# Optimization experiments

Measured on AMD Instinct MI355X. Metric: run time of the kernel, lower is better.

Reference implementation:

```python
import jax, jax.numpy as jnp
from jax import lax
import numpy as np

B, W, M, F = 8, 20, 512, 16
H = 128          # n_hidden
HALF = 64        # half_hid
K = 10           # conv out channels
LONG_K = W // 2  # dilated conv kernel


def setup_inputs() -> dict:
    key = jax.random.key(0)
    ks = jax.random.split(key, 24)
    s = 0.1  # weight scale (xavier-ish)
    return {
        "X": jax.random.normal(ks[0], (B, W, M, F), jnp.float32),
        "Y": jax.random.uniform(ks[1], (B, M), jnp.float32),
        "adj": jax.random.uniform(ks[2], (M, M), jnp.float32),
        "V": jax.random.normal(ks[3], (HALF,), jnp.float32) * s,
        "bv": jax.random.normal(ks[4], (1,), jnp.float32) * s,
        "W1": jax.random.normal(ks[5], (HALF, H), jnp.float32) * s,
        "b1": jax.random.normal(ks[6], (HALF,), jnp.float32) * s,
        "W2": jax.random.normal(ks[7], (HALF, H), jnp.float32) * s,
        "Wb": jax.random.normal(ks[8], (M, M), jnp.float32) * s,
        "wb": jax.random.normal(ks[9], (1,), jnp.float32) * s,
        "conv_w": jax.random.normal(ks[10], (K, F, W), jnp.float32) * s,
        "conv_b": jax.random.normal(ks[11], (K,), jnp.float32) * s,
        "convl_w": jax.random.normal(ks[12], (K, F, LONG_K), jnp.float32) * s,
        "convl_b": jax.random.normal(ks[13], (K,), jnp.float32) * s,
        "gru_Wih": jax.random.normal(ks[14], (3 * H, F), jnp.float32) * s,
        "gru_Whh": jax.random.normal(ks[15], (3 * H, H), jnp.float32) * s,
        "gru_bih": jax.random.normal(ks[16], (3 * H,), jnp.float32) * s,
        "gru_bhh": jax.random.normal(ks[17], (3 * H,), jnp.float32) * s,
        "gc1_W": jax.random.normal(ks[18], (3 * K, H), jnp.float32) * s,
        "gc1_b": jax.random.normal(ks[19], (H,), jnp.float32) * s,
        "gc2_W": jax.random.normal(ks[20], (H, K), jnp.float32) * s,
        "gc2_b": jax.random.normal(ks[21], (K,), jnp.float32) * s,
        "out_W": jax.random.normal(ks[22], (1, H + K), jnp.float32) * s,
        "out_b": jax.random.normal(ks[23], (1,), jnp.float32) * s,
    }


def _gru_last(xseq, Wih, Whh, bih, bhh):
    # xseq: (N, T, F) -> last hidden (N, H), PyTorch GRU gate order r,z,n
    n_hid = Whh.shape[1]
    def step(h, x_t):
        gx = x_t @ Wih.T + bih
        gh = h @ Whh.T + bhh
        xr, xz, xn = jnp.split(gx, 3, axis=-1)
        hr, hz, hn = jnp.split(gh, 3, axis=-1)
        r = jax.nn.sigmoid(xr + hr)
        z = jax.nn.sigmoid(xz + hz)
        n = jnp.tanh(xn + r * hn)
        return (1.0 - z) * n + z * h, None
    h0 = jnp.zeros((xseq.shape[0], n_hid), xseq.dtype)
    hT, _ = lax.scan(step, h0, jnp.moveaxis(xseq, 1, 0))
    return hT


def _forward(X, Y, adj, V, bv, W1, b1, W2, Wb, wb, conv_w, conv_b, convl_w,
             convl_b, gru_Wih, gru_Whh, gru_bih, gru_bhh, gc1_W, gc1_b,
             gc2_W, gc2_b, out_W, out_b):
    b, w, m, f = X.shape
    # ---- temporal branch: GRU per node ----
    x = jnp.transpose(X, (0, 2, 1, 3)).reshape(b * m, w, f)
    last_hid = _gru_last(x, gru_Wih, gru_Whh, gru_bih, gru_bhh).reshape(b, m, -1)
    out_temporal = last_hid
    # ---- attention-style adaptive adjacency ----
    # hid_rpt_m[b,i,j]=last_hid[b,j]; hid_rpt_w[b,i,j]=last_hid[b,i]
    p1 = jnp.einsum('bjh,kh->bjk', last_hid, W1)  # pairs with column index j
    p2 = jnp.einsum('bih,kh->bik', last_hid, W2)  # pairs with row index i
    pre = p1[:, None, :, :] + p2[:, :, None, :] + b1  # (b,m,m,half)
    a_mx = jnp.einsum('bijk,k->bij', jax.nn.elu(pre), V) + bv[0]
    # F.normalize(p=2, dim=1)
    nrm = jnp.sqrt(jnp.sum(a_mx * a_mx, axis=1, keepdims=True))
    a_mx = a_mx / jnp.maximum(nrm, 1e-12)
    # ---- per-node conv1d (vectorized over nodes) ----
    Xc = jnp.transpose(X, (0, 2, 3, 1)).reshape(b * m, f, w)  # (bm, f, w)
    dn = ('NCH', 'OIH', 'NCH')
    r = lax.conv_general_dilated(Xc, conv_w, (1,), 'VALID', dimension_numbers=dn)
    r = r + conv_b[None, :, None]                      # (bm, K, 1)
    rl = lax.conv_general_dilated(Xc, convl_w, (1,), 'VALID',
                                  rhs_dilation=(2,), dimension_numbers=dn)
    rl = rl + convl_b[None, :, None]                   # (bm, K, long_out)
    r_cat = jnp.concatenate([r, rl], axis=-1)          # (bm, K, 1+long_out)
    r_l = jax.nn.relu(r_cat.reshape(b, m, -1))         # (b, m, (1+long_out)*K)
    # ---- gate learned adjacency with fixed adjacency ----
    c = jax.nn.sigmoid(jnp.einsum('bij,jk->bik', a_mx, Wb) + wb[0])
    A = adj[None] * c + a_mx * (1.0 - c)               # (b,m,m)
    # ---- graph convolutions: out = A @ (x @ W) + b ----
    h1 = jax.nn.relu(jnp.einsum('bij,bjh->bih', A, r_l @ gc1_W) + gc1_b)
    out_spatial = jax.nn.relu(jnp.einsum('bij,bjh->bih', A, h1 @ gc2_W) + gc2_b)
    # ---- readout ----
    out = jnp.concatenate([out_spatial, out_temporal], axis=-1)
    out = (out @ out_W.T + out_b).squeeze(-1)          # (b, m)
    y = out.reshape(-1)
    Yf = Y.reshape(-1)
    # BCE with logits: softplus(y) - Y*y, averaged
    loss = jnp.mean(jax.nn.softplus(y) - Yf * y)
    return loss, jax.nn.sigmoid(y)


def reference(X, Y, adj, V, bv, W1, b1, W2, Wb, wb, conv_w, conv_b, convl_w,
              convl_b, gru_Wih, gru_Whh, gru_bih, gru_bhh, gc1_W, gc1_b,
              gc2_W, gc2_b, out_W, out_b):
    return _forward(X, Y, adj, V, bv, W1, b1, W2, Wb, wb, conv_w, conv_b,
                    convl_w, convl_b, gru_Wih, gru_Whh, gru_bih, gru_bhh,
                    gc1_W, gc1_b, gc2_W, gc2_b, out_W, out_b)
```

## Files before the change

kernel.cpp:

```cpp
#include <hip/hip_runtime.h>
#include <math.h>

#define Bn 8
#define Wn 20
#define Mn 512
#define Fn 16
#define Hn 128

typedef __attribute__((ext_vector_type(8))) short short8;
typedef __attribute__((ext_vector_type(4))) float f32x4;
typedef unsigned short ushort_t;

__device__ __forceinline__ float sigmoidf_(float x) {
  return 1.0f / (1.0f + __expf(-x));
}
__device__ __forceinline__ float tanhf_(float x) {
  float xx = fminf(fmaxf(x, -15.f), 15.f);
  float e = __expf(2.f * xx);
  return (e - 1.f) / (e + 1.f);
}
__device__ __forceinline__ float reluf_(float x) { return fmaxf(x, 0.f); }
__device__ __forceinline__ float eluf_(float x) {
  return (x > 0.f) ? x : (__expf(x) - 1.f);
}
__device__ __forceinline__ ushort_t bf16_rne(float v) {
  unsigned u = __float_as_uint(v);
  u += 0x7FFFu + ((u >> 16) & 1u);
  return (ushort_t)(u >> 16);
}
__device__ __forceinline__ float bf16_to_f(ushort_t b) {
  return __uint_as_float(((unsigned)b) << 16);
}
__device__ __forceinline__ void split8(const float v[8], short8& hi, short8& lo) {
#pragma unroll
  for (int j = 0; j < 8; ++j) {
    ushort_t h = bf16_rne(v[j]);
    hi[j] = (short)h;
    lo[j] = (short)bf16_rne(v[j] - bf16_to_f(h));
  }
}
__device__ __forceinline__ void load_gate_frags(
    const float* __restrict__ Whh, const float* __restrict__ Wih,
    int row, int quad, short8 fr[5][2]) {
  const float* wrow = Whh + (long)row * 128;
#pragma unroll
  for (int ks = 0; ks < 4; ++ks) {
    float v[8];
    float4 a4 = *(const float4*)&wrow[ks * 32 + quad * 8];
    float4 b4 = *(const float4*)&wrow[ks * 32 + quad * 8 + 4];
    v[0] = a4.x; v[1] = a4.y; v[2] = a4.z; v[3] = a4.w;
    v[4] = b4.x; v[5] = b4.y; v[6] = b4.z; v[7] = b4.w;
    split8(v, fr[ks][0], fr[ks][1]);
  }
  {
    float v[8] = {0.f, 0.f, 0.f, 0.f, 0.f, 0.f, 0.f, 0.f};
    if (quad < 2) {
      const float* xrow = Wih + (long)row * 16;
      float4 a4 = *(const float4*)&xrow[quad * 8];
      float4 b4 = *(const float4*)&xrow[quad * 8 + 4];
      v[0] = a4.x; v[1] = a4.y; v[2] = a4.z; v[3] = a4.w;
      v[4] = b4.x; v[5] = b4.y; v[6] = b4.z; v[7] = b4.w;
    }
    split8(v, fr[4][0], fr[4][1]);
  }
}

#define LDK 168
#define HSZ (16 * LDK)
__global__ __launch_bounds__(512, 1) void gru_kernel(
    const float* __restrict__ X, const float* __restrict__ Whh,
    const float* __restrict__ Wih, const float* __restrict__ bih,
    const float* __restrict__ bhh, const float* __restrict__ W1,
    const float* __restrict__ W2, const float* __restrict__ b1,
    float* __restrict__ last_hid, float* __restrict__ p1,
    float* __restrict__ p2, float* __restrict__ ssq,
    float* __restrict__ d_out) {
  const int tid = threadIdx.x;
  const int wave = tid >> 6;
  const int lane = tid & 63;
  const int quad = lane >> 4;
  const int jl = lane & 15;
  const int j0 = wave * 16;
  const int blk = blockIdx.x;
  const int b = blk >> 5;
  const int m0 = (blk & 31) * 16;

  if (blk < 8) ssq[blk * 512 + tid] = 0.f;
  if (blk == 0 && tid == 0) d_out[0] = 0.f;

  __shared__ __align__(16) ushort_t smem_hs[4 * HSZ];

  short8 frR[5][2], frZ[5][2], frN[5][2];
  load_gate_frags(Whh, Wih, wave * 16 + jl, quad, frR);
  load_gate_frags(Whh, Wih, 128 + wave * 16 + jl, quad, frZ);
  load_gate_frags(Whh, Wih, 256 + wave * 16 + jl, quad, frN);

  const float cr  = bih[j0 + jl] + bhh[j0 + jl];
  const float cz  = bih[128 + j0 + jl] + bhh[128 + j0 + jl];
  const float cnx = bih[256 + j0 + jl];
  const float cnh = bhh[256 + j0 + jl];

  for (int i = tid; i < 4 * HSZ; i += 512) smem_hs[i] = 0;

  const float* Xb = X + (long)b * (Wn * Mn * Fn) + (long)m0 * Fn;
  float x0 = 0.f;
  if (tid < 256) x0 = Xb[tid];
  __syncthreads();
  if (tid < 256) {
    int s = tid >> 4, f = tid & 15;
    ushort_t hb = bf16_rne(x0);
    smem_hs[0 * HSZ + s * LDK + 128 + f] = hb;
    smem_hs[2 * HSZ + s * LDK + 128 + f] = bf16_rne(x0 - bf16_to_f(hb));
  }
  __syncthreads();

  float hp[4] = {0.f, 0.f, 0.f, 0.f};

  for (int t = 0; t < Wn; ++t) {
    const int cur = t & 1, nxt = cur ^ 1;
    const int hiC = cur * HSZ, loC = (2 + cur) * HSZ;
    const int hiN = nxt * HSZ, loN = (2 + nxt) * HSZ;
    float xpre = 0.f;
    if (tid < 256 && t < Wn - 1) xpre = Xb[(long)(t + 1) * (Mn * Fn) + tid];

    f32x4 aR[2], aZ[2], aHN[2], aXN;
    aR[0] = aR[1] = aZ[0] = aZ[1] = aHN[0] = aHN[1] = aXN = (f32x4){0.f, 0.f, 0.f, 0.f};
#pragma unroll
    for (int ks = 0; ks < 5; ++ks) {
      const int p = ks & 1;
      short8 ah = *(const short8*)&smem_hs[hiC + jl * LDK + ks * 32 + quad * 8];
      short8 al = *(const short8*)&smem_hs[loC + jl * LDK + ks * 32 + quad * 8];
      aR[p] = __builtin_amdgcn_mfma_f32_16x16x32_bf16(ah, frR[ks][0], aR[p], 0, 0, 0);
      aR[p] = __builtin_amdgcn_mfma_f32_16x16x32_bf16(ah, frR[ks][1], aR[p], 0, 0, 0);
      aR[p] = __builtin_amdgcn_mfma_f32_16x16x32_bf16(al, frR[ks][0], aR[p], 0, 0, 0);
      aZ[p] = __builtin_amdgcn_mfma_f32_16x16x32_bf16(ah, frZ[ks][0], aZ[p], 0, 0, 0);
      aZ[p] = __builtin_amdgcn_mfma_f32_16x16x32_bf16(ah, frZ[ks][1], aZ[p], 0, 0, 0);
      aZ[p] = __builtin_amdgcn_mfma_f32_16x16x32_bf16(al, frZ[ks][0], aZ[p], 0, 0, 0);
      if (ks < 4) {
        aHN[p] = __builtin_amdgcn_mfma_f32_16x16x32_bf16(ah, frN[ks][0], aHN[p], 0, 0, 0);
        aHN[p] = __builtin_amdgcn_mfma_f32_16x16x32_bf16(ah, frN[ks][1], aHN[p], 0, 0, 0);
        aHN[p] = __builtin_amdgcn_mfma_f32_16x16x32_bf16(al, frN[ks][0], aHN[p], 0, 0, 0);
      } else {
        aXN = __builtin_amdgcn_mfma_f32_16x16x32_bf16(ah, frN[4][0], aXN, 0, 0, 0);
        aXN = __builtin_amdgcn_mfma_f32_16x16x32_bf16(ah, frN[4][1], aXN, 0, 0, 0);
        aXN = __builtin_amdgcn_mfma_f32_16x16x32_bf16(al, frN[4][0], aXN, 0, 0, 0);
      }
    }

#pragma unroll
    for (int reg = 0; reg < 4; ++reg) {
      float r = sigmoidf_(aR[0][reg] + aR[1][reg] + cr);
      float z = sigmoidf_(aZ[0][reg] + aZ[1][reg] + cz);
      float n = tanhf_(aXN[reg] + cnx + r * (aHN[0][reg] + aHN[1][reg] + cnh));
      float h = (1.f - z) * n + z * hp[reg];
      hp[reg] = h;
      int s = quad * 4 + reg;
      ushort_t hb = bf16_rne(h);
      smem_hs[hiN + s * LDK + j0 + jl] = hb;
      smem_hs[loN + s * LDK + j0 + jl] = bf16_rne(h - bf16_to_f(hb));
    }
    if (tid < 256 && t < Wn - 1) {
      int s = tid >> 4, f = tid & 15;
      ushort_t hb = bf16_rne(xpre);
      smem_hs[hiN + s * LDK + 128 + f] = hb;
      smem_hs[loN + s * LDK + 128 + f] = bf16_rne(xpre - bf16_to_f(hb));
    }
    __syncthreads();
  }

  float* hs_f = (float*)smem_hs;
#pragma unroll
  for (int reg = 0; reg < 4; ++reg) {
    int s = quad * 4 + reg;
    float h = hp[reg];
    last_hid[(long)(blk * 16 + s) * Hn + j0 + jl] = h;
    hs_f[s * 132 + j0 + jl] = h;
  }
  __syncthreads();
  {
    int k = tid & 63;
    int part = (tid >> 6) & 1;
    int sg = tid >> 7;
    const float* Wp = part ? W2 : W1;
    float a[4];
    float init = part ? 0.f : b1[k];
    a[0] = a[1] = a[2] = a[3] = init;
    for (int h = 0; h < 128; h += 4) {
      float4 w = *(const float4*)&Wp[k * 128 + h];
#pragma unroll
      for (int rr = 0; rr < 4; ++rr) {
        float4 q = *(const float4*)&hs_f[(sg * 4 + rr) * 132 + h];
        a[rr] += q.x * w.x + q.y * w.y + q.z * w.z + q.w * w.w;
      }
    }
    float* outp = part ? p2 : p1;
#pragma unroll
    for (int rr = 0; rr < 4; ++rr)
      outp[(long)(blk * 16 + sg * 4 + rr) * 64 + k] = a[rr];
  }
}

__global__ __launch_bounds__(256, 2) void mid_kernel(
    const float* __restrict__ X, const float* __restrict__ conv_w,
    const float* __restrict__ conv_b, const float* __restrict__ convl_w,
    const float* __restrict__ convl_b, const float* __restrict__ gc1_W,
    const float* __restrict__ p1, const float* __restrict__ p2,
    const float* __restrict__ V, const float* __restrict__ bv,
    const float* __restrict__ Wb, ushort_t* __restrict__ t1T_hi,
    ushort_t* __restrict__ t1T_lo, ushort_t* __restrict__ WbT_hi,
    ushort_t* __restrict__ WbT_lo, float* __restrict__ amx,
    float* __restrict__ ssq) {
  int tid = threadIdx.x, blk = blockIdx.x;
  __shared__ __align__(16) char sm[30720];

  {
    float* xs  = (float*)sm;
    float* cw  = (float*)(sm + 10240);
    float* clw = (float*)(sm + 23040);
    float* rs  = (float*)(sm + 29440);
    int n0 = blk * 8, b = n0 >> 9, m0 = n0 & 511;
    for (int idx = tid; idx < 3200; idx += 256) cw[idx] = conv_w[idx];
    for (int idx = tid; idx < 1600; idx += 256) clw[idx] = convl_w[idx];
    if (tid < 128) {
      for (int w = 0; w < 20; ++w)
        xs[tid * 20 + w] = X[((long)(b * 20 + w) * 512 + m0) * 16 + tid];
    }
    __syncthreads();
    if (tid < 80) {
      int s = tid / 10, k = tid % 10;
      float a0 = conv_b[k];
      float l0 = convl_b[k], l1 = convl_b[k];
      for (int f = 0; f < 16; ++f) {
        const float* xp = &xs[(s * 16 + f) * 20];
#pragma unroll
        for (int w = 0; w < 20; ++w) a0 = fmaf(xp[w], cw[k * 320 + f * 20 + w], a0);
#pragma unroll
        for (int q = 0; q < 10; ++q) {
          float wv = clw[k * 160 + f * 10 + q];
          l0 = fmaf(xp[2 * q], wv, l0);
          l1 = fmaf(xp[2 * q + 1], wv, l1);
        }
      }
      rs[s * 32 + k * 3 + 0] = reluf_(a0);
      rs[s * 32 + k * 3 + 1] = reluf_(l0);
      rs[s * 32 + k * 3 + 2] = reluf_(l1);
    }
    __syncthreads();
    if (tid < 128) {
      float w[30];
#pragma unroll
      for (int q = 0; q < 30; ++q) w[q] = gc1_W[q * 128 + tid];
      long base = ((long)b * 128 + tid) * 512 + m0;
#pragma unroll
      for (int s = 0; s < 8; ++s) {
        float a = 0.f;
#pragma unroll
        for (int q = 0; q < 30; ++q) a = fmaf(rs[s * 32 + q], w[q], a);
        ushort_t hb = bf16_rne(a);
        t1T_hi[base + s] = hb;
        t1T_lo[base + s] = bf16_rne(a - bf16_to_f(hb));
      }
    }
  }

  {
    float* p1s  = (float*)sm;
    float* p2s  = (float*)(sm + 8704);
    float* cred = (float*)(sm + 17408);
    float4 vreg[16];
#pragma unroll
    for (int q = 0; q < 16; ++q) vreg[q] = *(const float4*)&V[q * 4];
    float bvv = bv[0];
    int r0 = tid >> 4, c0 = tid & 15;

    for (int it = 0; it < 4; ++it) {
      int tile = blk * 4 + it;
      int bz = tile >> 8, ti = (tile >> 4) & 15, tj = tile & 15;
      int i0 = ti * 32, j0 = tj * 32;
      __syncthreads();
      {
        int rr = tid >> 3, cc = (tid & 7) * 8;
        *(float4*)&p1s[rr * 68 + cc]     = *(const float4*)&p1[(long)(bz * 512 + j0 + rr) * 64 + cc];
        *(float4*)&p1s[rr * 68 + cc + 4] = *(const float4*)&p1[(long)(bz * 512 + j0 + rr) * 64 + cc + 4];
        *(float4*)&p2s[rr * 68 + cc]     = *(const float4*)&p2[(long)(bz * 512 + i0 + rr) * 64 + cc];
        *(float4*)&p2s[rr * 68 + cc + 4] = *(const float4*)&p2[(long)(bz * 512 + i0 + rr) * 64 + cc + 4];
      }
      __syncthreads();
      float acc[2][2] = {{0.f, 0.f}, {0.f, 0.f}};
#pragma unroll 4
      for (int kq = 0; kq < 16; ++kq) {
        float4 a1 = *(const float4*)&p1s[c0 * 68 + kq * 4];
        float4 a2 = *(const float4*)&p1s[(c0 + 16) * 68 + kq * 4];
        float4 b1 = *(const float4*)&p2s[r0 * 68 + kq * 4];
        float4 b2 = *(const float4*)&p2s[(r0 + 16) * 68 + kq * 4];
        float4 vv = vreg[kq];
        acc[0][0] = fmaf(eluf_(a1.x + b1.x), vv.x, acc[0][0]);
        acc[0][1] = fmaf(eluf_(a2.x + b1.x), vv.x, acc[0][1]);
        acc[1][0] = fmaf(eluf_(a1.x + b2.x), vv.x, acc[1][0]);
        acc[1][1] = fmaf(eluf_(a2.x + b2.x), vv.x, acc[1][1]);
        acc[0][0] = fmaf(eluf_(a1.y + b1.y), vv.y, acc[0][0]);
        acc[0][1] = fmaf(eluf_(a2.y + b1.y), vv.y, acc[0][1]);
        acc[1][0] = fmaf(eluf_(a1.y + b2.y), vv.y, acc[1][0]);
        acc[1][1] = fmaf(eluf_(a2.y + b2.y), vv.y, acc[1][1]);
        acc[0][0] = fmaf(eluf_(a1.z + b1.z), vv.z, acc[0][0]);
        acc[0][1] = fmaf(eluf_(a2.z + b1.z), vv.z, acc[0][1]);
        acc[1][0] = fmaf(eluf_(a1.z + b2.z), vv.z, acc[1][0]);
        acc[1][1] = fmaf(eluf_(a2.z + b2.z), vv.z, acc[1][1]);
        acc[0][0] = fmaf(eluf_(a1.w + b1.w), vv.w, acc[0][0]);
        acc[0][1] = fmaf(eluf_(a2.w + b1.w), vv.w, acc[0][1]);
        acc[1][0] = fmaf(eluf_(a1.w + b2.w), vv.w, acc[1][0]);
        acc[1][1] = fmaf(eluf_(a2.w + b2.w), vv.w, acc[1][1]);
      }
      float s2[2] = {0.f, 0.f};
#pragma unroll
      for (int aa = 0; aa < 2; ++aa)
#pragma unroll
        for (int cc = 0; cc < 2; ++cc) {
          float v = acc[aa][cc] + bvv;
          amx[((long)(bz * 512 + i0 + r0 + aa * 16)) * 512 + j0 + c0 + cc * 16] = v;
          s2[cc] += v * v;
        }
      cred[r0 * 33 + c0] = s2[0];
      cred[r0 * 33 + c0 + 16] = s2[1];
      __syncthreads();
      if (tid < 32) {
        float s = 0.f;
#pragma unroll
        for (int p = 0; p < 16; ++p) s += cred[p * 33 + tid];
        atomicAdd(&ssq[bz * 512 + j0 + tid], s);
      }
    }
  }

  if (blk < 64) {
    __syncthreads();
    float* wt = (float*)sm;
    int k0 = (blk >> 3) * 64, j0w = (blk & 7) * 64;
    for (int idx = tid; idx < 4096; idx += 256) {
      int r = idx >> 6, c = idx & 63;
      wt[r * 65 + c] = Wb[(long)(k0 + r) * 512 + j0w + c];
    }
    __syncthreads();
    for (int idx = tid; idx < 4096; idx += 256) {
      int r = idx >> 6, c = idx & 63;
      float v = wt[c * 65 + r];
      ushort_t hb = bf16_rne(v);
      WbT_hi[(long)(j0w + r) * 512 + k0 + c] = hb;
      WbT_lo[(long)(j0w + r) * 512 + k0 + c] = bf16_rne(v - bf16_to_f(hb));
    }
  }
}

#define CPK 40
__global__ __launch_bounds__(256, 2) void gemm_cA(
    const float* __restrict__ amx, const ushort_t* __restrict__ WbT_hi,
    const ushort_t* __restrict__ WbT_lo, const float* __restrict__ adj,
    const float* __restrict__ wb, const float* __restrict__ ssq,
    float* __restrict__ A) {
  const int bz = blockIdx.z;
  const int i0 = blockIdx.y * 64;
  const int j0 = blockIdx.x * 64;
  const int tid = threadIdx.x;
  const int wave = tid >> 6;
  const int lane = tid & 63;
  const int quad = lane >> 4, jl = lane & 15;
  const int wm = (wave & 1) * 32, wn = (wave >> 1) * 32;

  __shared__ __align__(16) ushort_t Ahi[64][CPK];
  __shared__ __align__(16) ushort_t Alo[64][CPK];
  __shared__ __align__(16) ushort_t Bhi[64][CPK];
  __shared__ __align__(16) ushort_t Blo[64][CPK];
  __shared__ float rs_s[512];

  const float* Abase = amx + (long)bz * 262144;
  const float* sb = ssq + bz * 512;
  for (int i = tid; i < 512; i += 256)
    rs_s[i] = 1.f / fmaxf(sqrtf(sb[i]), 1e-12f);

  f32x4 acc[2][2];
#pragma unroll
  for (int a = 0; a < 2; ++a)
#pragma unroll
    for (int c = 0; c < 2; ++c) acc[a][c] = (f32x4){0.f, 0.f, 0.f, 0.f};

  for (int kk0 = 0; kk0 < 512; kk0 += 32) {
    __syncthreads();
#pragma unroll
    for (int l = 0; l < 2; ++l) {
      int e = l * 1024 + tid * 4;
      int r = e >> 5, kq = e & 31;
      float4 v = *(const float4*)&Abase[(long)(i0 + r) * 512 + kk0 + kq];
      float4 sc = *(const float4*)&rs_s[kk0 + kq];
      float vv[4] = {v.x * sc.x, v.y * sc.y, v.z * sc.z, v.w * sc.w};
#pragma unroll
      for (int q = 0; q < 4; ++q) {
        ushort_t hb = bf16_rne(vv[q]);
        Ahi[r][kq + q] = hb;
        Alo[r][kq + q] = bf16_rne(vv[q] - bf16_to_f(hb));
      }
    }
    {
      int r = tid >> 2, kc = (tid & 3) * 8;
      *(uint4*)&Bhi[r][kc] = *(const uint4*)&WbT_hi[(long)(j0 + r) * 512 + kk0 + kc];
      *(uint4*)&Blo[r][kc] = *(const uint4*)&WbT_lo[(long)(j0 + r) * 512 + kk0 + kc];
    }
    __syncthreads();
    short8 ah[2], al[2], bh[2], bl[2];
#pragma unroll
    for (int tm = 0; tm < 2; ++tm) {
      ah[tm] = *(const short8*)&Ahi[wm + tm * 16 + jl][quad * 8];
      al[tm] = *(const short8*)&Alo[wm + tm * 16 + jl][quad * 8];
    }
#pragma unroll
    for (int tn = 0; tn < 2; ++tn) {
      bh[tn] = *(const short8*)&Bhi[wn + tn * 16 + jl][quad * 8];
      bl[tn] = *(const short8*)&Blo[wn + tn * 16 + jl][quad * 8];
    }
#pragma unroll
    for (int tm = 0; tm < 2; ++tm)
#pragma unroll
      for (int tn = 0; tn < 2; ++tn) {
        acc[tm][tn] = __builtin_amdgcn_mfma_f32_16x16x32_bf16(ah[tm], bh[tn], acc[tm][tn], 0, 0, 0);
        acc[tm][tn] = __builtin_amdgcn_mfma_f32_16x16x32_bf16(ah[tm], bl[tn], acc[tm][tn], 0, 0, 0);
        acc[tm][tn] = __builtin_amdgcn_mfma_f32_16x16x32_bf16(al[tm], bh[tn], acc[tm][tn], 0, 0, 0);
      }
  }

  const float wbv = wb[0];
#pragma unroll
  for (int tn = 0; tn < 2; ++tn) {
    int j = j0 + wn + tn * 16 + jl;
    float sj = rs_s[j];
#pragma unroll
    for (int tm = 0; tm < 2; ++tm) {
#pragma unroll
      for (int reg = 0; reg < 4; ++reg) {
        int i = i0 + wm + tm * 16 + quad * 4 + reg;
        long ofs = (long)bz * 262144 + (long)i * 512 + j;
        float c = sigmoidf_(acc[tm][tn][reg] + wbv);
        float am = Abase[(long)i * 512 + j] * sj;
        float ad = adj[(long)i * 512 + j];
        A[ofs] = ad * c + am * (1.f - c);
      }
    }
  }
}

__global__ __launch_bounds__(512, 1) void gemm_h1t2(
    const float* __restrict__ A, const ushort_t* __restrict__ t1T_hi,
    const ushort_t* __restrict__ t1T_lo, const float* __restrict__ gc1_b,
    const float* __restrict__ gc2_W, float* __restrict__ t2) {
  const int bz = blockIdx.y;
  const int i0 = blockIdx.x * 16;
  const int tid = threadIdx.x;
  const int wave = tid >> 6;
  const int lane = tid & 63;
  const int quad = lane >> 4, jl = lane & 15;

  __shared__ __align__(16) ushort_t Ahi[16][CPK];
  __shared__ __align__(16) ushort_t Alo[16][CPK];
  __shared__ __align__(16) ushort_t Bhi[128][CPK];
  __shared__ __align__(16) ushort_t Blo[128][CPK];
  __shared__ float h1s[16][132];
  __shared__ float gw[1280];

  const float* Ab = A + (long)bz * 262144;
  for (int idx = tid; idx < 1280; idx += 512) gw[idx] = gc2_W[idx];

  f32x4 acc = {0.f, 0.f, 0.f, 0.f};

  for (int kk0 = 0; kk0 < 512; kk0 += 32) {
    __syncthreads();
    {
      int r = tid >> 5, kq = tid & 31;
      float v = Ab[(long)(i0 + r) * 512 + kk0 + kq];
      ushort_t hb = bf16_rne(v);
      Ahi[r][kq] = hb;
      Alo[r][kq] = bf16_rne(v - bf16_to_f(hb));
    }
    {
      int r = tid >> 2, kc = (tid & 3) * 8;
      *(uint4*)&Bhi[r][kc] = *(const uint4*)&t1T_hi[((long)bz * 128 + r) * 512 + kk0 + kc];
      *(uint4*)&Blo[r][kc] = *(const uint4*)&t1T_lo[((long)bz * 128 + r) * 512 + kk0 + kc];
    }
    __syncthreads();
    short8 ah = *(const short8*)&Ahi[jl][quad * 8];
    short8 al = *(const short8*)&Alo[jl][quad * 8];
    short8 bh = *(const short8*)&Bhi[wave * 16 + jl][quad * 8];
    short8 bl = *(const short8*)&Blo[wave * 16 + jl][quad * 8];
    acc = __builtin_amdgcn_mfma_f32_16x16x32_bf16(ah, bh, acc, 0, 0, 0);
    acc = __builtin_amdgcn_mfma_f32_16x16x32_bf16(ah, bl, acc, 0, 0, 0);
    acc = __builtin_amdgcn_mfma_f32_16x16x32_bf16(al, bh, acc, 0, 0, 0);
  }
  __syncthreads();
  {
    int n = wave * 16 + jl;
    float bb = gc1_b[n];
#pragma unroll
    for (int reg = 0; reg < 4; ++reg) {
      int r = quad * 4 + reg;
      h1s[r][n] = reluf_(acc[reg] + bb);
    }
  }
  __syncthreads();
  if (tid < 160) {
    int r = tid / 10, c = tid % 10;
    float a = 0.f;
#pragma unroll 4
    for (int k = 0; k < 128; ++k) a = fmaf(h1s[r][k], gw[k * 10 + c], a);
    t2[((long)bz * 512 + i0 + r) * 10 + c] = a;
  }
}

__global__ __launch_bounds__(256) void spat_readout(
    const float* __restrict__ A, const float* __restrict__ t2,
    const float* __restrict__ gc2_b, const float* __restrict__ last_hid,
    const float* __restrict__ out_W, const float* __restrict__ out_b,
    const float* __restrict__ Y, float* __restrict__ d_out) {
  int tid = threadIdx.x;
  int bz = blockIdx.y;
  int i0 = blockIdx.x * 8;
  __shared__ float t2s[5120];
  __shared__ float wS[138];
  __shared__ float osps[8][12];
  for (int idx = tid; idx < 5120; idx += 256) t2s[idx] = t2[(long)bz * 5120 + idx];
  for (int idx = tid; idx < 138; idx += 256) wS[idx] = out_W[idx];
  __syncthreads();
  int r = tid >> 5, sk = tid & 31;
  const float* Arow = A + (long)bz * 262144 + (long)(i0 + r) * 512;
  float acc[10] = {0, 0, 0, 0, 0, 0, 0, 0, 0, 0};
  for (int k = sk; k < 512; k += 32) {
    float av = Arow[k];
    const float* tp = &t2s[k * 10];
#pragma unroll
    for (int c = 0; c < 10; ++c) acc[c] = fmaf(av, tp[c], acc[c]);
  }
#pragma unroll
  for (int off = 16; off; off >>= 1)
#pragma unroll
    for (int c = 0; c < 10; ++c) acc[c] += __shfl_xor(acc[c], off);
  if (sk == 0) {
#pragma unroll
    for (int c = 0; c < 10; ++c) osps[r][c] = reluf_(acc[c] + gc2_b[c]);
  }
  __syncthreads();
  float l = 0.f;
  if (tid < 8) {
    int gid = bz * 512 + i0 + tid;
    float y = out_b[0];
#pragma unroll
    for (int k = 0; k < 10; ++k) y = fmaf(osps[tid][k], wS[k], y);
    const float* hp = &last_hid[(long)gid * 128];
    for (int h = 0; h < 128; h += 4) {
      float4 hv = *(const float4*)&hp[h];
      y = fmaf(hv.x, wS[10 + h + 0], y);
      y = fmaf(hv.y, wS[10 + h + 1], y);
      y = fmaf(hv.z, wS[10 + h + 2], y);
      y = fmaf(hv.w, wS[10 + h + 3], y);
    }
    d_out[1 + gid] = sigmoidf_(y);
    l = fmaxf(y, 0.f) + log1pf(__expf(-fabsf(y))) - Y[gid] * y;
  }
  if (tid < 64) {
#pragma unroll
    for (int off = 4; off; off >>= 1) l += __shfl_down(l, off);
    if (tid == 0) atomicAdd(d_out, l * (1.0f / 4096.f));
  }
}

extern "C" void kernel_launch(void* const* d_in, const int* in_sizes, int n_in,
                              void* d_out, int out_size, void* d_ws, size_t ws_size,
                              hipStream_t stream) {
  const float* X       = (const float*)d_in[0];
  const float* Y       = (const float*)d_in[1];
  const float* adj     = (const float*)d_in[2];
  const float* V       = (const float*)d_in[3];
  const float* bv      = (const float*)d_in[4];
  const float* W1      = (const float*)d_in[5];
  const float* b1      = (const float*)d_in[6];
  const float* W2      = (const float*)d_in[7];
  const float* Wb      = (const float*)d_in[8];
  const float* wb      = (const float*)d_in[9];
  const float* conv_w  = (const float*)d_in[10];
  const float* conv_b  = (const float*)d_in[11];
  const float* convl_w = (const float*)d_in[12];
  const float* convl_b = (const float*)d_in[13];
  const float* gWih    = (const float*)d_in[14];
  const float* gWhh    = (const float*)d_in[15];
  const float* gbih    = (const float*)d_in[16];
  const float* gbhh    = (const float*)d_in[17];
  const float* gc1_W   = (const float*)d_in[18];
  const float* gc1_b   = (const float*)d_in[19];
  const float* gc2_W   = (const float*)d_in[20];
  const float* gc2_b   = (const float*)d_in[21];
  const float* out_W   = (const float*)d_in[22];
  const float* out_b   = (const float*)d_in[23];
  float* out = (float*)d_out;

  float* ws = (float*)d_ws;
  float* lhid  = ws; ws += 524288;
  float* p1    = ws; ws += 262144;
  float* p2    = ws; ws += 262144;
  float* amx   = ws; ws += 2097152;
  float* ssq   = ws; ws += 4096;
  float* Abuf  = ws; ws += 2097152;
  float* t2    = ws; ws += 40960;
  float* WbTf  = ws; ws += 262144;
  float* t1Tf  = ws; ws += 524288;
  if (ws_size < (size_t)(ws - (float*)d_ws) * sizeof(float)) return;
  ushort_t* WbT_hi = (ushort_t*)WbTf;
  ushort_t* WbT_lo = WbT_hi + 262144;
  ushort_t* t1T_hi = (ushort_t*)t1Tf;
  ushort_t* t1T_lo = t1T_hi + 524288;

  gru_kernel<<<256, 512, 0, stream>>>(X, gWhh, gWih, gbih, gbhh, W1, W2, b1,
                                      lhid, p1, p2, ssq, out);
  mid_kernel<<<512, 256, 0, stream>>>(X, conv_w, conv_b, convl_w, convl_b,
                                      gc1_W, p1, p2, V, bv, Wb,
                                      t1T_hi, t1T_lo, WbT_hi, WbT_lo, amx, ssq);
  gemm_cA<<<dim3(8, 8, 8), 256, 0, stream>>>(amx, WbT_hi, WbT_lo, adj, wb,
                                             ssq, Abuf);
  gemm_h1t2<<<dim3(32, 8), 512, 0, stream>>>(Abuf, t1T_hi, t1T_lo, gc1_b,
                                             gc2_W, t2);
  spat_readout<<<dim3(64, 8), 256, 0, stream>>>(Abuf, t2, gc2_b, lhid,
                                                out_W, out_b, Y, out);
}
```

Before: 258.4 us.

## Enlarge attention-score tile to 64x64 per block and use fast reciprocals

The additive attention score computation in mid_kernel now gives each block one 64x64 tile with a 4x4 register tile per thread, replacing four 32x32 tiles with 2x2 per thread. This cuts shared-memory reloads of p1/p2 and the per-tile syncs and atomics, and raises arithmetic reuse per LDS load. Shared memory grows and register pressure rises. Sigmoid, tanh and the inverse-norm computation also switch to the hardware approximate reciprocal, which slightly loosens accuracy.

```diff
diff --git a/kernel.cpp b/kernel.cpp
--- a/kernel.cpp
+++ b/kernel.cpp
@@ -12,12 +12,13 @@
 typedef unsigned short ushort_t;
 
 __device__ __forceinline__ float sigmoidf_(float x) {
-  return 1.0f / (1.0f + __expf(-x));
+  float e = __expf(-x);
+  return __builtin_amdgcn_rcpf(1.0f + e);
 }
 __device__ __forceinline__ float tanhf_(float x) {
   float xx = fminf(fmaxf(x, -15.f), 15.f);
   float e = __expf(2.f * xx);
-  return (e - 1.f) / (e + 1.f);
+  return (e - 1.f) * __builtin_amdgcn_rcpf(e + 1.f);
 }
 __device__ __forceinline__ float reluf_(float x) { return fmaxf(x, 0.f); }
 __device__ __forceinline__ float eluf_(float x) {
@@ -211,7 +212,7 @@
     ushort_t* __restrict__ WbT_lo, float* __restrict__ amx,
     float* __restrict__ ssq) {
   int tid = threadIdx.x, blk = blockIdx.x;
-  __shared__ __align__(16) char sm[30720];
+  __shared__ __align__(16) char sm[39168];
 
   {
     float* xs  = (float*)sm;
@@ -262,73 +263,65 @@
       }
     }
   }
+  __syncthreads();
 
   {
     float* p1s  = (float*)sm;
-    float* p2s  = (float*)(sm + 8704);
-    float* cred = (float*)(sm + 17408);
+    float* p2s  = (float*)(sm + 17408);
+    float* cred = (float*)(sm + 34816);
     float4 vreg[16];
 #pragma unroll
     for (int q = 0; q < 16; ++q) vreg[q] = *(const float4*)&V[q * 4];
     float bvv = bv[0];
+    int bz = blk >> 6, i0 = ((blk >> 3) & 7) * 64, j0 = (blk & 7) * 64;
     int r0 = tid >> 4, c0 = tid & 15;
 
-    for (int it = 0; it < 4; ++it) {
-      int tile = blk * 4 + it;
-      int bz = tile >> 8, ti = (tile >> 4) & 15, tj = tile & 15;
-      int i0 = ti * 32, j0 = tj * 32;
-      __syncthreads();
-      {
-        int rr = tid >> 3, cc = (tid & 7) * 8;
-        *(float4*)&p1s[rr * 68 + cc]     = *(const float4*)&p1[(long)(bz * 512 + j0 + rr) * 64 + cc];
-        *(float4*)&p1s[rr * 68 + cc + 4] = *(const float4*)&p1[(long)(bz * 512 + j0 + rr) * 64 + cc + 4];
-        *(float4*)&p2s[rr * 68 + cc]     = *(const float4*)&p2[(long)(bz * 512 + i0 + rr) * 64 + cc];
-        *(float4*)&p2s[rr * 68 + cc + 4] = *(const float4*)&p2[(long)(bz * 512 + i0 + rr) * 64 + cc + 4];
-      }
-      __syncthreads();
-      float acc[2][2] = {{0.f, 0.f}, {0.f, 0.f}};
-#pragma unroll 4
-      for (int kq = 0; kq < 16; ++kq) {
-        float4 a1 = *(const float4*)&p1s[c0 * 68 + kq * 4];
-        float4 a2 = *(const float4*)&p1s[(c0 + 16) * 68 + kq * 4];
-        float4 b1 = *(const float4*)&p2s[r0 * 68 + kq * 4];
-        float4 b2 = *(const float4*)&p2s[(r0 + 16) * 68 + kq * 4];
-        float4 vv = vreg[kq];
-        acc[0][0] = fmaf(eluf_(a1.x + b1.x), vv.x, acc[0][0]);
-        acc[0][1] = fmaf(eluf_(a2.x + b1.x), vv.x, acc[0][1]);
-        acc[1][0] = fmaf(eluf_(a1.x + b2.x), vv.x, acc[1][0]);
-        acc[1][1] = fmaf(eluf_(a2.x + b2.x), vv.x, acc[1][1]);
-        acc[0][0] = fmaf(eluf_(a1.y + b1.y), vv.y, acc[0][0]);
-        acc[0][1] = fmaf(eluf_(a2.y + b1.y), vv.y, acc[0][1]);
-        acc[1][0] = fmaf(eluf_(a1.y + b2.y), vv.y, acc[1][0]);
-        acc[1][1] = fmaf(eluf_(a2.y + b2.y), vv.y, acc[1][1]);
-        acc[0][0] = fmaf(eluf_(a1.z + b1.z), vv.z, acc[0][0]);
-        acc[0][1] = fmaf(eluf_(a2.z + b1.z), vv.z, acc[0][1]);
-        acc[1][0] = fmaf(eluf_(a1.z + b2.z), vv.z, acc[1][0]);
-        acc[1][1] = fmaf(eluf_(a2.z + b2.z), vv.z, acc[1][1]);
-        acc[0][0] = fmaf(eluf_(a1.w + b1.w), vv.w, acc[0][0]);
-        acc[0][1] = fmaf(eluf_(a2.w + b1.w), vv.w, acc[0][1]);
-        acc[1][0] = fmaf(eluf_(a1.w + b2.w), vv.w, acc[1][0]);
-        acc[1][1] = fmaf(eluf_(a2.w + b2.w), vv.w, acc[1][1]);
-      }
-      float s2[2] = {0.f, 0.f};
-#pragma unroll
-      for (int aa = 0; aa < 2; ++aa)
-#pragma unroll
-        for (int cc = 0; cc < 2; ++cc) {
-          float v = acc[aa][cc] + bvv;
-          amx[((long)(bz * 512 + i0 + r0 + aa * 16)) * 512 + j0 + c0 + cc * 16] = v;
-          s2[cc] += v * v;
+#pragma unroll
+    for (int l = 0; l < 4; ++l) {
+      int e = l * 1024 + tid * 4;
+      int r = e >> 6, c = e & 63;
+      *(float4*)&p1s[r * 68 + c] = *(const float4*)&p1[(long)(bz * 512 + j0 + r) * 64 + c];
+      *(float4*)&p2s[r * 68 + c] = *(const float4*)&p2[(long)(bz * 512 + i0 + r) * 64 + c];
+    }
+    __syncthreads();
+
+    float acc[4][4] = {};
+    for (int kq = 0; kq < 16; ++kq) {
+      float4 pa[4], pb[4];
+#pragma unroll
+      for (int q = 0; q < 4; ++q) {
+        pa[q] = *(const float4*)&p1s[(c0 + q * 16) * 68 + kq * 4];
+        pb[q] = *(const float4*)&p2s[(r0 + q * 16) * 68 + kq * 4];
+      }
+      float4 vv = vreg[kq];
+#pragma unroll
+      for (int ri = 0; ri < 4; ++ri)
+#pragma unroll
+        for (int ci = 0; ci < 4; ++ci) {
+          acc[ri][ci] = fmaf(eluf_(pa[ci].x + pb[ri].x), vv.x, acc[ri][ci]);
+          acc[ri][ci] = fmaf(eluf_(pa[ci].y + pb[ri].y), vv.y, acc[ri][ci]);
+          acc[ri][ci] = fmaf(eluf_(pa[ci].z + pb[ri].z), vv.z, acc[ri][ci]);
+          acc[ri][ci] = fmaf(eluf_(pa[ci].w + pb[ri].w), vv.w, acc[ri][ci]);
         }
-      cred[r0 * 33 + c0] = s2[0];
-      cred[r0 * 33 + c0 + 16] = s2[1];
-      __syncthreads();
-      if (tid < 32) {
-        float s = 0.f;
-#pragma unroll
-        for (int p = 0; p < 16; ++p) s += cred[p * 33 + tid];
-        atomicAdd(&ssq[bz * 512 + j0 + tid], s);
-      }
+    }
+    float s2[4] = {0.f, 0.f, 0.f, 0.f};
+#pragma unroll
+    for (int ri = 0; ri < 4; ++ri)
+#pragma unroll
+      for (int ci = 0; ci < 4; ++ci) {
+        float v = acc[ri][ci] + bvv;
+        amx[((long)(bz * 512 + i0 + r0 + ri * 16)) * 512 + j0 + c0 + ci * 16] = v;
+        s2[ci] += v * v;
+      }
+    __syncthreads();
+#pragma unroll
+    for (int ci = 0; ci < 4; ++ci) cred[r0 * 68 + c0 + ci * 16] = s2[ci];
+    __syncthreads();
+    if (tid < 64) {
+      float s = 0.f;
+#pragma unroll
+      for (int p = 0; p < 16; ++p) s += cred[p * 68 + tid];
+      atomicAdd(&ssq[bz * 512 + j0 + tid], s);
     }
   }
 
@@ -375,7 +368,7 @@
   const float* Abase = amx + (long)bz * 262144;
   const float* sb = ssq + bz * 512;
   for (int i = tid; i < 512; i += 256)
-    rs_s[i] = 1.f / fmaxf(sqrtf(sb[i]), 1e-12f);
+    rs_s[i] = __builtin_amdgcn_rcpf(fmaxf(sqrtf(sb[i]), 1e-12f));
 
   f32x4 acc[2][2];
 #pragma unroll
```

New measurement: 246.7 us. 4.5% less time.
